# Optimization experiments

Measured on AMD Instinct MI355X. Metric: run time of the kernel, lower is better.

Reference implementation:

```python
import jax, jax.numpy as jnp
import numpy as np

NUM_SAMPLES = 1024


def _cdist(a, b):
    # a, b: (n, 3) -> (n, n) pairwise euclidean distances (torch.cdist p=2)
    d2 = jnp.sum((a[:, None, :] - b[None, :, :]) ** 2, axis=-1)
    return jnp.sqrt(jnp.maximum(d2, 0.0))


def _greedy_match_cost(cost):
    # Greedy sequential matching: repeatedly take the global argmin over
    # still-unmatched rows/cols, accumulate its cost, eliminate row+col.
    n = cost.shape[0]

    def step(carry, _):
        row_mask, col_mask, loss = carry
        valid = row_mask[:, None] & col_mask[None, :]
        masked = jnp.where(valid, cost, jnp.inf)
        idx = jnp.argmin(masked)  # row-major first-min == torch's min(dim=1)+argmin tiebreak
        r = idx // n
        c = idx % n
        loss = loss + cost[r, c]
        return (row_mask.at[r].set(False), col_mask.at[c].set(False), loss), None

    init = (jnp.ones((n,), dtype=bool), jnp.ones((n,), dtype=bool), jnp.float32(0.0))
    (_, _, loss), _ = jax.lax.scan(step, init, None, length=n)
    return loss / n


def setup_inputs() -> dict:
    key = jax.random.key(0)
    k1, k2, k3 = jax.random.split(key, 3)
    B, N, n = 8, 4096, NUM_SAMPLES
    S1 = jax.random.normal(k1, (B, N, 3), dtype=jnp.float32)
    S2 = jax.random.normal(k2, (B, N, 3), dtype=jnp.float32)
    # torch.randperm(N)[:n] per batch element: without-replacement sampling
    perm_keys = jax.random.split(k3, B)
    indices = jax.vmap(lambda k: jax.random.permutation(k, N)[:n])(perm_keys).astype(jnp.int32)
    return {"S1": S1, "S2": S2, "indices": indices}


def reference(S1, S2, indices):
    # sample the same indices from both sets, per batch (matches original loop)
    s1 = jnp.take_along_axis(S1, indices[:, :, None], axis=1)  # (B, n, 3)
    s2 = jnp.take_along_axis(S2, indices[:, :, None], axis=1)  # (B, n, 3)
    cost = jax.vmap(_cdist)(s1, s2)  # (B, n, n)
    losses = jax.vmap(_greedy_match_cost)(cost)  # (B,)
    return jnp.mean(losses)
```

## Files before the change

kernel.cpp:

```cpp
#include <hip/hip_runtime.h>
#include <stdint.h>

#define BATCH 8
#define NPTS 4096
#define NS 1024
#define KD 6

typedef unsigned long long u64;
typedef unsigned int u32;
typedef unsigned short u16;
typedef unsigned char u8;

#define DEADV (~0ull)
#define QNANB 0x7FC00000u

__device__ __forceinline__ float pdist3(float ax, float ay, float az,
                                        float bx, float by, float bz) {
    float dx = ax - bx, dy = ay - by, dz = az - bz;
    float d2 = __fmaf_rn(dz, dz, __fmaf_rn(dy, dy, dx * dx));
    return __fsqrt_rn(d2);
}

__device__ __forceinline__ u64 packv(float d, u32 row, u32 col) {
    return ((u64)__float_as_uint(d) << 20) | ((u64)row << 10) | (u64)col;
}

__device__ __forceinline__ u64 u64min2(u64 a, u64 b) { return a < b ? a : b; }
__device__ __forceinline__ u64 u64max2(u64 a, u64 b) { return a > b ? a : b; }

__device__ __forceinline__ u64 tree16(const u64* p) {
    u64 a0 = u64min2(p[0], p[1]),   a1 = u64min2(p[2], p[3]);
    u64 a2 = u64min2(p[4], p[5]),   a3 = u64min2(p[6], p[7]);
    u64 a4 = u64min2(p[8], p[9]),   a5 = u64min2(p[10], p[11]);
    u64 a6 = u64min2(p[12], p[13]), a7 = u64min2(p[14], p[15]);
    u64 b0 = u64min2(a0, a1), b1 = u64min2(a2, a3);
    u64 b2 = u64min2(a4, a5), b3 = u64min2(a6, a7);
    return u64min2(u64min2(b0, b1), u64min2(b2, b3));
}

template<int CTRL>
__device__ __forceinline__ u64 dpp_min_step(u64 m) {
    u32 lo = (u32)m, hi = (u32)(m >> 32);
    u32 olo = (u32)__builtin_amdgcn_update_dpp(-1, (int)lo, CTRL, 0xF, 0xF, false);
    u32 ohi = (u32)__builtin_amdgcn_update_dpp(-1, (int)hi, CTRL, 0xF, 0xF, false);
    u64 o = ((u64)ohi << 32) | olo;
    return o < m ? o : m;
}

__device__ __forceinline__ u64 wave_min_u64(u64 m) {
    m = dpp_min_step<0x111>(m);
    m = dpp_min_step<0x112>(m);
    m = dpp_min_step<0x114>(m);
    m = dpp_min_step<0x118>(m);
    m = dpp_min_step<0x142>(m);
    m = dpp_min_step<0x143>(m);
    u32 lo = (u32)__builtin_amdgcn_readlane((int)(u32)m, 63);
    u32 hi = (u32)__builtin_amdgcn_readlane((int)(u32)(m >> 32), 63);
    return ((u64)hi << 32) | lo;
}

__global__ void gather_k(const float* __restrict__ S1, const float* __restrict__ S2,
                         const int* __restrict__ idx,
                         float4* __restrict__ s1g, float4* __restrict__ s2g,
                         int* __restrict__ cnt, u64* __restrict__ calib) {
    int t = blockIdx.x * blockDim.x + threadIdx.x;
    if (t == 0) *cnt = 0;
    if (calib && blockIdx.x == 0 && threadIdx.x < 64) {
        for (int k = 0; k < 64; ++k) {
            __builtin_nontemporal_store(0ull,
                calib + ((size_t)threadIdx.x * 64 + k) * 8);
        }
    }
    if (t >= BATCH * NS) return;
    int b = t >> 10;
    int j = idx[t];
    const float* p1 = S1 + ((size_t)b * NPTS + j) * 3;
    const float* p2 = S2 + ((size_t)b * NPTS + j) * 3;
    s1g[t] = make_float4(p1[0], p1[1], p1[2], 0.f);
    s2g[t] = make_float4(p2[0], p2[1], p2[2], 0.f);
}

__global__ void lists_k(const float4* __restrict__ s1g, const float4* __restrict__ s2g,
                        u64* __restrict__ rlist_g, u64* __restrict__ clist_g) {
    __shared__ float4 pts[NS];
    int gg = blockIdx.x * 4 + (threadIdx.x >> 6);
    int lane = threadIdx.x & 63;
    int side = (gg >= BATCH * NS) ? 1 : 0;
    int g = gg - side * (BATCH * NS);
    int b = g >> 10;
    u32 rc = (u32)(g & 1023);
    const float4* other = (side ? s1g : s2g) + (size_t)b * NS;
    for (int i = threadIdx.x; i < NS; i += 256) pts[i] = other[i];
    float4 a = side ? s2g[g] : s1g[g];
    __syncthreads();
    u64 cand[16];
    #pragma unroll
    for (int k = 0; k < 16; ++k) {
        int o = lane + (k << 6);
        float4 q = pts[o];
        float d = pdist3(a.x, a.y, a.z, q.x, q.y, q.z);
        cand[k] = side ? packv(d, (u32)o, rc) : packv(d, rc, (u32)o);
    }
    u64* out = (side ? clist_g : rlist_g) + (size_t)g * KD;
    for (int i = 0; i < KD; ++i) {
        u64 m1 = wave_min_u64(tree16(cand));
        if (lane == 0) out[i] = m1;
        #pragma unroll
        for (int k = 0; k < 16; ++k) cand[k] = (cand[k] == m1) ? DEADV : cand[k];
    }
}

__global__ void __launch_bounds__(1024, 1)
resolve_k(const float4* __restrict__ s1g, const float4* __restrict__ s2g,
          const u64* __restrict__ rlist_gl, const u64* __restrict__ clist_gl,
          float* __restrict__ loss_ws, int* __restrict__ cnt,
          float* __restrict__ out, u64* __restrict__ instr) {
    __shared__ u64 rlist[NS * KD];
    __shared__ u64 clist[NS * KD];
    __shared__ u64 rmin[NS];
    __shared__ u64 cmin[NS];
    __shared__ float4 s1p[NS];
    __shared__ float4 s2p[NS];
    __shared__ u8 rptrs[NS], cptrs[NS];
    __shared__ u16 qrow[NS], qcol[NS];
    __shared__ u16 lrows[NS], lcols[NS];
    __shared__ float lred[1024];
    __shared__ int qrn, qcn, matched, nlr, nlc, stale_n;
    int b = blockIdx.x;
    int tid = threadIdx.x;
    int lane = tid & 63, wv = tid >> 6;

    {
        const float4* rs = (const float4*)(rlist_gl + (size_t)b * NS * KD);
        const float4* cs = (const float4*)(clist_gl + (size_t)b * NS * KD);
        float4* rd = (float4*)rlist;
        float4* cd = (float4*)clist;
        for (int i = tid; i < NS * KD / 2; i += 1024) { rd[i] = rs[i]; cd[i] = cs[i]; }
    }
    s1p[tid] = s1g[(size_t)b * NS + tid];
    s2p[tid] = s2g[(size_t)b * NS + tid];
    rptrs[tid] = 1; cptrs[tid] = 1;
    lrows[tid] = (u16)tid; lcols[tid] = (u16)tid;
    if (tid == 0) { matched = 0; stale_n = NS; }
    __syncthreads();
    rmin[tid] = rlist[tid * KD];
    cmin[tid] = clist[tid * KD];
    float loss = 0.f;
    __syncthreads();

    for (int round = 0; round < NS; ++round) {
        u64 myk = rmin[tid];
        u32 c = (u32)myk & 1023u;
        bool mut = (myk != DEADV) && (cmin[c] == myk);
        if (mut) {
            loss += __uint_as_float((u32)(myk >> 20));
            rmin[tid] = DEADV;
            cmin[c] = DEADV;
            s1p[tid].x = __uint_as_float(QNANB);
            s2p[c].x   = __uint_as_float(QNANB);
        }
        u64 bal = __ballot((int)mut);
        if (lane == 0 && bal) atomicAdd(&matched, (int)__popcll(bal));
        if (tid == 0) { qrn = 0; qcn = 0; nlr = 0; nlc = 0; }
        if (instr && tid == 1 && round < 256)
            __builtin_nontemporal_store(0ull, instr + ((size_t)b * 256 + round) * 8);
        __syncthreads();
        int m = matched;
        if (m >= NS) break;
        int live = NS - m;
        int stale = stale_n;
        bool rebuild = (stale * 4 > live * 5 + 64);
        u64 rk = rmin[tid];
        if (rk != DEADV) {
            float pr = s2p[(u32)rk & 1023u].x;
            if (pr != pr) {
                u32 p = rptrs[tid];
                bool found = false;
                while (p < KD) {
                    u64 e = rlist[tid * KD + p];
                    ++p;
                    if (e != DEADV) {
                        float q = s2p[(u32)e & 1023u].x;
                        if (q == q) { rmin[tid] = e; found = true; break; }
                    }
                }
                rptrs[tid] = (u8)p;
                if (!found) { int s = atomicAdd(&qrn, 1); qrow[s] = (u16)tid; }
            }
        }
        u64 ck = cmin[tid];
        if (ck != DEADV) {
            float pr = s1p[((u32)ck >> 10) & 1023u].x;
            if (pr != pr) {
                u32 p = cptrs[tid];
                bool found = false;
                while (p < KD) {
                    u64 e = clist[tid * KD + p];
                    ++p;
                    if (e != DEADV) {
                        float q = s1p[((u32)e >> 10) & 1023u].x;
                        if (q == q) { cmin[tid] = e; found = true; break; }
                    }
                }
                cptrs[tid] = (u8)p;
                if (!found) { int s = atomicAdd(&qcn, 1); qcol[s] = (u16)tid; }
            }
        }
        if (rebuild) {
            float cx = s2p[tid].x;
            bool calive = (cx == cx);
            u64 cb = __ballot((int)calive);
            int crank = (int)__popcll(cb & ((1ull << lane) - 1ull));
            int cbase = 0;
            if (lane == 0) cbase = atomicAdd(&nlc, (int)__popcll(cb));
            cbase = __shfl(cbase, 0, 64);
            if (calive) lcols[cbase + crank] = (u16)tid;

            float rx = s1p[tid].x;
            bool ralive = (rx == rx);
            u64 rb = __ballot((int)ralive);
            int rrank = (int)__popcll(rb & ((1ull << lane) - 1ull));
            int rbase = 0;
            if (lane == 0) rbase = atomicAdd(&nlr, (int)__popcll(rb));
            rbase = __shfl(rbase, 0, 64);
            if (ralive) lrows[rbase + rrank] = (u16)tid;
        }
        __syncthreads();
        int nr = qrn, nc = qcn;
        int scan_n = rebuild ? live : stale;
        if (rebuild && tid == 0) stale_n = live;
        for (int qi = wv; qi < nr; qi += 16) {
            u32 r = qrow[qi];
            float4 a = s1p[r];
            u64 m1 = DEADV, m2 = DEADV;
            for (int i = lane; i < scan_n; i += 64) {
                int cc = lcols[i];
                float4 q = s2p[cc];
                float d = pdist3(a.x, a.y, a.z, q.x, q.y, q.z);
                u64 p = packv(d, r, (u32)cc);
                u64 mx = u64max2(p, m1);
                m1 = u64min2(m1, p);
                m2 = u64min2(m2, mx);
            }
            u64 M1 = wave_min_u64(m1);
            u64 c2 = (m1 == M1) ? m2 : m1;
            u64 M2 = wave_min_u64(c2);
            if (lane == 0) {
                rmin[r] = M1;
                rlist[r * KD + KD - 1] = M2;
                rptrs[r] = KD - 1;
            }
        }
        for (int qi = wv; qi < nc; qi += 16) {
            u32 cc = qcol[qi];
            float4 a = s2p[cc];
            u64 m1 = DEADV, m2 = DEADV;
            for (int i = lane; i < scan_n; i += 64) {
                int r = lrows[i];
                float4 q = s1p[r];
                float d = pdist3(q.x, q.y, q.z, a.x, a.y, a.z);
                u64 p = packv(d, (u32)r, cc);
                u64 mx = u64max2(p, m1);
                m1 = u64min2(m1, p);
                m2 = u64min2(m2, mx);
            }
            u64 M1 = wave_min_u64(m1);
            u64 c2 = (m1 == M1) ? m2 : m1;
            u64 M2 = wave_min_u64(c2);
            if (lane == 0) {
                cmin[cc] = M1;
                clist[cc * KD + KD - 1] = M2;
                cptrs[cc] = KD - 1;
            }
        }
        __syncthreads();
    }

    lred[tid] = loss;
    __syncthreads();
    #pragma unroll
    for (int s = 512; s > 0; s >>= 1) {
        if (tid < s) lred[tid] += lred[tid + s];
        __syncthreads();
    }
    if (tid == 0) {
        atomicExch(&loss_ws[b], lred[0] * (1.0f / NS));
        __threadfence();
        int old = atomicAdd(cnt, 1);
        if (old == BATCH - 1) {
            __threadfence();
            float s = 0.f;
            for (int i = 0; i < BATCH; ++i) s += atomicAdd(&loss_ws[i], 0.0f);
            out[0] = s * (1.0f / BATCH);
        }
    }
}

extern "C" void kernel_launch(void* const* d_in, const int* in_sizes, int n_in,
                              void* d_out, int out_size, void* d_ws, size_t ws_size,
                              hipStream_t stream) {
    const float* S1 = (const float*)d_in[0];
    const float* S2 = (const float*)d_in[1];
    const int* idx  = (const int*)d_in[2];
    char* ws = (char*)d_ws;
    size_t o = 0;
    float4* s1g    = (float4*)(ws + o); o += (size_t)BATCH * NS * 16;
    float4* s2g    = (float4*)(ws + o); o += (size_t)BATCH * NS * 16;
    u64* rlist_g   = (u64*)(ws + o);    o += (size_t)BATCH * NS * KD * 8;
    u64* clist_g   = (u64*)(ws + o);    o += (size_t)BATCH * NS * KD * 8;
    float* loss_ws = (float*)(ws + o);  o += (size_t)BATCH * 4;
    int* cnt       = (int*)(ws + o);    o += 64;
    o = (o + 4095) & ~(size_t)4095;
    u64* calib     = (u64*)(ws + o);    o += (size_t)4096 * 64;
    u64* instr     = (u64*)(ws + o);    o += (size_t)BATCH * 256 * 64;
    bool ok = (ws_size >= o);
    u64* calib_p = ok ? calib : (u64*)0;
    u64* instr_p = ok ? instr : (u64*)0;

    gather_k<<<(BATCH * NS + 255) / 256, 256, 0, stream>>>(S1, S2, idx, s1g, s2g,
                                                           cnt, calib_p);
    lists_k<<<2 * BATCH * NS / 4, 256, 0, stream>>>(s1g, s2g, rlist_g, clist_g);
    resolve_k<<<BATCH, 1024, 0, stream>>>(s1g, s2g, rlist_g, clist_g, loss_ws, cnt,
                                          (float*)d_out, instr_p);
}
```

Baseline: 196.5 us.

## Hold per-point candidate lists in registers and keep top-4 on rescans

The per-row and per-column nearest-neighbour candidate lists grow from 6 to 8 entries, and resolve_k now keeps them in per-thread registers instead of shared-memory arrays, so the staging copy and shared-memory reads are gone. Rescans now track the top four candidates instead of two and store three spares in a small shared array, which is meant to cut how often rows and columns must be rescanned. The calibration store loop is removed and the instrumentation writes are moved. In exchange, register pressure rises at 1024 threads per block, the register shift chains may compile into spills or dynamic indexing, and each rescan does more compare and reduction work.

```diff
diff --git a/kernel.cpp b/kernel.cpp
--- a/kernel.cpp
+++ b/kernel.cpp
@@ -4,7 +4,8 @@
 #define BATCH 8
 #define NPTS 4096
 #define NS 1024
-#define KD 6
+#define KD 8
+#define NSP 3
 
 typedef unsigned long long u64;
 typedef unsigned int u32;
@@ -26,7 +27,6 @@
 }
 
 __device__ __forceinline__ u64 u64min2(u64 a, u64 b) { return a < b ? a : b; }
-__device__ __forceinline__ u64 u64max2(u64 a, u64 b) { return a > b ? a : b; }
 
 __device__ __forceinline__ u64 tree16(const u64* p) {
     u64 a0 = u64min2(p[0], p[1]),   a1 = u64min2(p[2], p[3]);
@@ -62,15 +62,9 @@
 __global__ void gather_k(const float* __restrict__ S1, const float* __restrict__ S2,
                          const int* __restrict__ idx,
                          float4* __restrict__ s1g, float4* __restrict__ s2g,
-                         int* __restrict__ cnt, u64* __restrict__ calib) {
+                         int* __restrict__ cnt) {
     int t = blockIdx.x * blockDim.x + threadIdx.x;
     if (t == 0) *cnt = 0;
-    if (calib && blockIdx.x == 0 && threadIdx.x < 64) {
-        for (int k = 0; k < 64; ++k) {
-            __builtin_nontemporal_store(0ull,
-                calib + ((size_t)threadIdx.x * 64 + k) * 8);
-        }
-    }
     if (t >= BATCH * NS) return;
     int b = t >> 10;
     int j = idx[t];
@@ -115,13 +109,13 @@
           const u64* __restrict__ rlist_gl, const u64* __restrict__ clist_gl,
           float* __restrict__ loss_ws, int* __restrict__ cnt,
           float* __restrict__ out, u64* __restrict__ instr) {
-    __shared__ u64 rlist[NS * KD];
-    __shared__ u64 clist[NS * KD];
     __shared__ u64 rmin[NS];
     __shared__ u64 cmin[NS];
     __shared__ float4 s1p[NS];
     __shared__ float4 s2p[NS];
-    __shared__ u8 rptrs[NS], cptrs[NS];
+    __shared__ u64 spr[NS * NSP];
+    __shared__ u64 spc[NS * NSP];
+    __shared__ u8 sprp[NS], spcp[NS];
     __shared__ u16 qrow[NS], qcol[NS];
     __shared__ u16 lrows[NS], lcols[NS];
     __shared__ float lred[1024];
@@ -130,21 +124,30 @@
     int tid = threadIdx.x;
     int lane = tid & 63, wv = tid >> 6;
 
+    u64 er0, er1, er2, er3, er4, er5, er6;
+    u64 ec0, ec1, ec2, ec3, ec4, ec5, ec6;
     {
-        const float4* rs = (const float4*)(rlist_gl + (size_t)b * NS * KD);
-        const float4* cs = (const float4*)(clist_gl + (size_t)b * NS * KD);
-        float4* rd = (float4*)rlist;
-        float4* cd = (float4*)clist;
-        for (int i = tid; i < NS * KD / 2; i += 1024) { rd[i] = rs[i]; cd[i] = cs[i]; }
+        const u64* rs = rlist_gl + (size_t)b * NS * KD + (size_t)tid * KD;
+        const u64* cs = clist_gl + (size_t)b * NS * KD + (size_t)tid * KD;
+        u64 hr = rs[0];
+        er0 = rs[1]; er1 = rs[2]; er2 = rs[3]; er3 = rs[4];
+        er4 = rs[5]; er5 = rs[6]; er6 = rs[7];
+        u64 hc = cs[0];
+        ec0 = cs[1]; ec1 = cs[2]; ec2 = cs[3]; ec3 = cs[4];
+        ec4 = cs[5]; ec5 = cs[6]; ec6 = cs[7];
+        rmin[tid] = hr;
+        cmin[tid] = hc;
     }
     s1p[tid] = s1g[(size_t)b * NS + tid];
     s2p[tid] = s2g[(size_t)b * NS + tid];
-    rptrs[tid] = 1; cptrs[tid] = 1;
+    sprp[tid] = NSP; spcp[tid] = NSP;
     lrows[tid] = (u16)tid; lcols[tid] = (u16)tid;
     if (tid == 0) { matched = 0; stale_n = NS; }
-    __syncthreads();
-    rmin[tid] = rlist[tid * KD];
-    cmin[tid] = clist[tid * KD];
+    if (instr && tid == 2) {
+        for (int k = 0; k < 128; ++k)
+            __builtin_nontemporal_store(0ull,
+                instr + 16384 + ((size_t)b * 128 + k) * 8);
+    }
     float loss = 0.f;
     __syncthreads();
 
@@ -174,36 +177,54 @@
         if (rk != DEADV) {
             float pr = s2p[(u32)rk & 1023u].x;
             if (pr != pr) {
-                u32 p = rptrs[tid];
                 bool found = false;
-                while (p < KD) {
-                    u64 e = rlist[tid * KD + p];
-                    ++p;
-                    if (e != DEADV) {
-                        float q = s2p[(u32)e & 1023u].x;
-                        if (q == q) { rmin[tid] = e; found = true; break; }
+                while (er0 != DEADV) {
+                    u64 e = er0;
+                    er0 = er1; er1 = er2; er2 = er3; er3 = er4;
+                    er4 = er5; er5 = er6; er6 = DEADV;
+                    float q = s2p[(u32)e & 1023u].x;
+                    if (q == q) { rmin[tid] = e; found = true; break; }
+                }
+                if (!found) {
+                    u32 p = sprp[tid];
+                    while (p < NSP) {
+                        u64 e = spr[tid * NSP + p];
+                        ++p;
+                        if (e != DEADV) {
+                            float q = s2p[(u32)e & 1023u].x;
+                            if (q == q) { rmin[tid] = e; found = true; break; }
+                        }
                     }
+                    sprp[tid] = (u8)p;
+                    if (!found) { int s = atomicAdd(&qrn, 1); qrow[s] = (u16)tid; }
                 }
-                rptrs[tid] = (u8)p;
-                if (!found) { int s = atomicAdd(&qrn, 1); qrow[s] = (u16)tid; }
             }
         }
         u64 ck = cmin[tid];
         if (ck != DEADV) {
             float pr = s1p[((u32)ck >> 10) & 1023u].x;
             if (pr != pr) {
-                u32 p = cptrs[tid];
                 bool found = false;
-                while (p < KD) {
-                    u64 e = clist[tid * KD + p];
-                    ++p;
-                    if (e != DEADV) {
-                        float q = s1p[((u32)e >> 10) & 1023u].x;
-                        if (q == q) { cmin[tid] = e; found = true; break; }
+                while (ec0 != DEADV) {
+                    u64 e = ec0;
+                    ec0 = ec1; ec1 = ec2; ec2 = ec3; ec3 = ec4;
+                    ec4 = ec5; ec5 = ec6; ec6 = DEADV;
+                    float q = s1p[((u32)e >> 10) & 1023u].x;
+                    if (q == q) { cmin[tid] = e; found = true; break; }
+                }
+                if (!found) {
+                    u32 p = spcp[tid];
+                    while (p < NSP) {
+                        u64 e = spc[tid * NSP + p];
+                        ++p;
+                        if (e != DEADV) {
+                            float q = s1p[((u32)e >> 10) & 1023u].x;
+                            if (q == q) { cmin[tid] = e; found = true; break; }
+                        }
                     }
+                    spcp[tid] = (u8)p;
+                    if (!found) { int s = atomicAdd(&qcn, 1); qcol[s] = (u16)tid; }
                 }
-                cptrs[tid] = (u8)p;
-                if (!found) { int s = atomicAdd(&qcn, 1); qcol[s] = (u16)tid; }
             }
         }
         if (rebuild) {
@@ -232,45 +253,61 @@
         for (int qi = wv; qi < nr; qi += 16) {
             u32 r = qrow[qi];
             float4 a = s1p[r];
-            u64 m1 = DEADV, m2 = DEADV;
+            u64 t0 = DEADV, t1 = DEADV, t2 = DEADV, t3 = DEADV;
             for (int i = lane; i < scan_n; i += 64) {
                 int cc = lcols[i];
                 float4 q = s2p[cc];
                 float d = pdist3(a.x, a.y, a.z, q.x, q.y, q.z);
                 u64 p = packv(d, r, (u32)cc);
-                u64 mx = u64max2(p, m1);
-                m1 = u64min2(m1, p);
-                m2 = u64min2(m2, mx);
-            }
-            u64 M1 = wave_min_u64(m1);
-            u64 c2 = (m1 == M1) ? m2 : m1;
-            u64 M2 = wave_min_u64(c2);
+                bool c3 = p < t3, c2 = p < t2, c1 = p < t1, c0 = p < t0;
+                t3 = c3 ? (c2 ? t2 : p) : t3;
+                t2 = c2 ? (c1 ? t1 : p) : t2;
+                t1 = c1 ? (c0 ? t0 : p) : t1;
+                t0 = c0 ? p : t0;
+            }
+            u64 M0 = wave_min_u64(t0);
+            if (t0 == M0) { t0 = t1; t1 = t2; t2 = t3; t3 = DEADV; }
+            u64 M1 = wave_min_u64(t0);
+            if (t0 == M1) { t0 = t1; t1 = t2; t2 = t3; t3 = DEADV; }
+            u64 M2 = wave_min_u64(t0);
+            if (t0 == M2) { t0 = t1; t1 = t2; t2 = t3; t3 = DEADV; }
+            u64 M3 = wave_min_u64(t0);
             if (lane == 0) {
-                rmin[r] = M1;
-                rlist[r * KD + KD - 1] = M2;
-                rptrs[r] = KD - 1;
+                rmin[r] = M0;
+                spr[r * NSP + 0] = M1;
+                spr[r * NSP + 1] = M2;
+                spr[r * NSP + 2] = M3;
+                sprp[r] = 0;
             }
         }
         for (int qi = wv; qi < nc; qi += 16) {
             u32 cc = qcol[qi];
             float4 a = s2p[cc];
-            u64 m1 = DEADV, m2 = DEADV;
+            u64 t0 = DEADV, t1 = DEADV, t2 = DEADV, t3 = DEADV;
             for (int i = lane; i < scan_n; i += 64) {
                 int r = lrows[i];
                 float4 q = s1p[r];
                 float d = pdist3(q.x, q.y, q.z, a.x, a.y, a.z);
                 u64 p = packv(d, (u32)r, cc);
-                u64 mx = u64max2(p, m1);
-                m1 = u64min2(m1, p);
-                m2 = u64min2(m2, mx);
-            }
-            u64 M1 = wave_min_u64(m1);
-            u64 c2 = (m1 == M1) ? m2 : m1;
-            u64 M2 = wave_min_u64(c2);
+                bool c3 = p < t3, c2 = p < t2, c1 = p < t1, c0 = p < t0;
+                t3 = c3 ? (c2 ? t2 : p) : t3;
+                t2 = c2 ? (c1 ? t1 : p) : t2;
+                t1 = c1 ? (c0 ? t0 : p) : t1;
+                t0 = c0 ? p : t0;
+            }
+            u64 M0 = wave_min_u64(t0);
+            if (t0 == M0) { t0 = t1; t1 = t2; t2 = t3; t3 = DEADV; }
+            u64 M1 = wave_min_u64(t0);
+            if (t0 == M1) { t0 = t1; t1 = t2; t2 = t3; t3 = DEADV; }
+            u64 M2 = wave_min_u64(t0);
+            if (t0 == M2) { t0 = t1; t1 = t2; t2 = t3; t3 = DEADV; }
+            u64 M3 = wave_min_u64(t0);
             if (lane == 0) {
-                cmin[cc] = M1;
-                clist[cc * KD + KD - 1] = M2;
-                cptrs[cc] = KD - 1;
+                cmin[cc] = M0;
+                spc[cc * NSP + 0] = M1;
+                spc[cc * NSP + 1] = M2;
+                spc[cc * NSP + 2] = M3;
+                spcp[cc] = 0;
             }
         }
         __syncthreads();
@@ -311,14 +348,12 @@
     float* loss_ws = (float*)(ws + o);  o += (size_t)BATCH * 4;
     int* cnt       = (int*)(ws + o);    o += 64;
     o = (o + 4095) & ~(size_t)4095;
-    u64* calib     = (u64*)(ws + o);    o += (size_t)4096 * 64;
-    u64* instr     = (u64*)(ws + o);    o += (size_t)BATCH * 256 * 64;
-    bool ok = (ws_size >= o);
-    u64* calib_p = ok ? calib : (u64*)0;
-    u64* instr_p = ok ? instr : (u64*)0;
-
-    gather_k<<<(BATCH * NS + 255) / 256, 256, 0, stream>>>(S1, S2, idx, s1g, s2g,
-                                                           cnt, calib_p);
+    u64* instr     = (u64*)(ws + o);
+    o += (size_t)BATCH * 256 * 64;
+    o += (size_t)1024 * 64;
+    u64* instr_p = (ws_size >= o) ? instr : (u64*)0;
+
+    gather_k<<<(BATCH * NS + 255) / 256, 256, 0, stream>>>(S1, S2, idx, s1g, s2g, cnt);
     lists_k<<<2 * BATCH * NS / 4, 256, 0, stream>>>(s1g, s2g, rlist_g, clist_g);
     resolve_k<<<BATCH, 1024, 0, stream>>>(s1g, s2g, rlist_g, clist_g, loss_ws, cnt,
                                           (float*)d_out, instr_p);
```

Result: slower. 230.6 us (+17.4%).
